# Kernel optimization log

Hardware: AMD Instinct MI355X
Metric: run time of the kernel (lower is better)

Reference implementation:

```python
import jax, jax.numpy as jnp
import numpy as np

EMBED_DIM = 1024
NUM_HEADS = 16
D_K = EMBED_DIM // NUM_HEADS
GAMMA = 1.0


def setup_inputs() -> dict:
    key = jax.random.key(0)
    ks = jax.random.split(key, 5)
    B, N, E = 2, 2048, EMBED_DIM
    scale = 1.0 / np.sqrt(E)
    x = jax.random.normal(ks[0], (B, N, E), dtype=jnp.float32)
    Wq = jax.random.normal(ks[1], (E, E), dtype=jnp.float32) * scale
    Wk = jax.random.normal(ks[2], (E, E), dtype=jnp.float32) * scale
    Wv = jax.random.normal(ks[3], (E, E), dtype=jnp.float32) * scale
    Wo = jax.random.normal(ks[4], (E, E), dtype=jnp.float32) * scale
    mask = jnp.ones((B, N), dtype=jnp.int32)
    return {"x": x, "Wq": Wq, "Wk": Wk, "Wv": Wv, "Wo": Wo, "mask": mask}


def _split_heads(t):
    B, N, E = t.shape
    return t.reshape(B, N, NUM_HEADS, D_K).transpose(0, 2, 1, 3)  # [B,H,N,dk]


def reference(x, Wq, Wk, Wv, Wo, mask):
    B, N, E = x.shape
    # Linear layers (bias=False): y = x @ W.T
    q = _split_heads(x @ Wq.T)
    k = _split_heads(x @ Wk.T)
    v = _split_heads(x @ Wv.T)
    # Squared L2 distance via ||q||^2 + ||k||^2 - 2 q.k (same math as (q-k)^2.sum,
    # without materializing the [B,H,N,N,dk] diff tensor).
    q_sq = jnp.sum(q * q, axis=-1)  # [B,H,N]
    k_sq = jnp.sum(k * k, axis=-1)  # [B,H,N]
    qk = jnp.einsum('bhqd,bhkd->bhqk', q, k)
    sq_dist = jnp.maximum(q_sq[..., :, None] + k_sq[..., None, :] - 2.0 * qk, 0.0)
    similarity = jnp.exp(-GAMMA * sq_dist)  # [B,H,N,N]
    # mask.unsqueeze(1).unsqueeze(2): broadcast over heads and query dim
    mask_exp = mask[:, None, None, :]  # [B,1,1,N]
    similarity = jnp.where(mask_exp == 0, jnp.float32(-1e9), similarity)
    attn = jax.nn.softmax(similarity, axis=-1)
    # dropout p=0.0 (eval) -> identity
    out = jnp.einsum('bhqk,bhkd->bhqd', attn, v)
    out = out.transpose(0, 2, 1, 3).reshape(B, N, E)
    return out @ Wo.T
```

## Files before the change

kernel.cpp:

```cpp
#include <hip/hip_runtime.h>
#include <hip/hip_bf16.h>


using bf16x8 = __attribute__((ext_vector_type(8))) __bf16;
using f32x4  = __attribute__((ext_vector_type(4))) float;
using f32x16 = __attribute__((ext_vector_type(16))) float;

typedef const __attribute__((address_space(1))) void* gas_t;
typedef __attribute__((address_space(3))) void* las_t;

#define C_LOG2E 1.4426950408889634f
#define TWO_C   2.8853900817779268f
#define NEG_INV_4C (-0.17328679513998632f)

#if __has_builtin(__builtin_amdgcn_exp2f)
#define EXP2(x) __builtin_amdgcn_exp2f(x)
#else
#define EXP2(x) __expf((x) * 0.6931471805599453f)
#endif

static __device__ __forceinline__ unsigned short f2bf(float x) {
  union { float f; unsigned u; } c; c.f = x;
  unsigned u = c.u;
  u += 0x7fffu + ((u >> 16) & 1u);
  return (unsigned short)(u >> 16);
}
static __device__ __forceinline__ float bf2f(unsigned short b) {
  union { unsigned u; float f; } c; c.u = ((unsigned)b) << 16;
  return c.f;
}
static __device__ __forceinline__ unsigned cvt_pk_bf16(float lo, float hi) {
  unsigned r;
  asm("v_cvt_pk_bf16_f32 %0, %1, %2" : "=v"(r) : "v"(lo), "v"(hi));
  return r;
}
static __device__ __forceinline__ void permlane32_swap(unsigned &a, unsigned &b) {
#if __has_builtin(__builtin_amdgcn_permlane32_swap)
  auto r = __builtin_amdgcn_permlane32_swap(a, b, false, false);
  a = r[0]; b = r[1];
#else
  asm("v_permlane32_swap_b32 %0, %1" : "+v"(a), "+v"(b));
#endif
}

__global__ __launch_bounds__(256)
void cvt_all(const float* __restrict__ x,  const float* __restrict__ wq,
             const float* __restrict__ wk, const float* __restrict__ wv,
             const float* __restrict__ wo,
             unsigned short* __restrict__ xbf, unsigned short* __restrict__ Wbf) {
  const int idx = blockIdx.x * 256 + threadIdx.x;
  const float* src; unsigned short* dst; int off;
  if (idx < 1048576) { src = x; dst = xbf; off = idx; }
  else {
    const int r = idx - 1048576;
    const int w = r >> 18;
    off = r & 262143;
    src = (w == 0) ? wq : (w == 1) ? wk : (w == 2) ? wv : wo;
    dst = Wbf + (size_t)w * 1048576u;
  }
  const float4 v = ((const float4*)src)[off];
  ushort4 o;
  o.x = f2bf(v.x); o.y = f2bf(v.y); o.z = f2bf(v.z); o.w = f2bf(v.w);
  ((ushort4*)dst)[off] = o;
}

__global__ __launch_bounds__(256)
void gemm_bt(const unsigned short* __restrict__ A,
             const unsigned short* __restrict__ Bt,
             void* __restrict__ out0, int Kdim, int mode) {
  __shared__ unsigned short As[2][4096];
  __shared__ unsigned short Bs[2][4096];
  const int t  = threadIdx.x;
  const int m0 = blockIdx.x * 128;
  const int n0 = blockIdx.y * 128;
  const int srow = t >> 2;
  const int scol = (t & 3) * 8;
  const unsigned short* pA = A  + (size_t)(m0 + srow) * Kdim + scol;
  const unsigned short* pB = Bt + (size_t)(n0 + srow) * Kdim + scol;
  const size_t rowskip = (size_t)64 * Kdim;

  const int wave = t >> 6, lane = t & 63;
  const int wm = (wave >> 1) * 64, wn = (wave & 1) * 64;
  const int fr = lane & 15, fg = lane >> 4;
  const int aoff = (wm + fr) * 32 + fg * 8;
  const int boff = (wn + fr) * 32 + fg * 8;

  f32x4 acc[4][4];
#pragma unroll
  for (int mi = 0; mi < 4; ++mi)
#pragma unroll
    for (int ni = 0; ni < 4; ++ni)
      acc[mi][ni] = (f32x4){0.f, 0.f, 0.f, 0.f};

#define GSTAGE(bi, kk)                                                                                  \
  do {                                                                                                  \
    const int kc = (kk) * 32;                                                                           \
    __builtin_amdgcn_global_load_lds((gas_t)(const void*)(pA + kc),           (las_t)(void*)(As[bi] + t * 8),        16, 0, 0); \
    __builtin_amdgcn_global_load_lds((gas_t)(const void*)(pA + kc + rowskip), (las_t)(void*)(As[bi] + 2048 + t * 8), 16, 0, 0); \
    __builtin_amdgcn_global_load_lds((gas_t)(const void*)(pB + kc),           (las_t)(void*)(Bs[bi] + t * 8),        16, 0, 0); \
    __builtin_amdgcn_global_load_lds((gas_t)(const void*)(pB + kc + rowskip), (las_t)(void*)(Bs[bi] + 2048 + t * 8), 16, 0, 0); \
  } while (0)

  const int NK = Kdim >> 5;
  GSTAGE(0, 0);
  __syncthreads();

  for (int ks = 0; ks < NK; ++ks) {
    const int cur = ks & 1;
    if (ks + 1 < NK) GSTAGE(cur ^ 1, ks + 1);

    bf16x8 af[4], bfr[4];
#pragma unroll
    for (int mi = 0; mi < 4; ++mi) af[mi]  = *(const bf16x8*)(As[cur] + aoff + mi * 512);
#pragma unroll
    for (int ni = 0; ni < 4; ++ni) bfr[ni] = *(const bf16x8*)(Bs[cur] + boff + ni * 512);
#pragma unroll
    for (int mi = 0; mi < 4; ++mi)
#pragma unroll
      for (int ni = 0; ni < 4; ++ni)
        acc[mi][ni] = __builtin_amdgcn_mfma_f32_16x16x32_bf16(af[mi], bfr[ni], acc[mi][ni], 0, 0, 0);
    __syncthreads();
  }
#undef GSTAGE

#pragma unroll
  for (int mi = 0; mi < 4; ++mi) {
    const int gm = m0 + wm + mi * 16 + fg * 4;
#pragma unroll
    for (int ni = 0; ni < 4; ++ni) {
      const int gn = n0 + wn + ni * 16 + fr;
      if (mode == 0) {
        unsigned short* outw = (unsigned short*)out0;
        const int z = gn >> 10, col = gn & 1023;
        if (z < 2) {
          const float sc = (z == 0) ? TWO_C : 1.0f;
          unsigned short* dst = outw + (size_t)z * 4194304u;
#pragma unroll
          for (int r = 0; r < 4; ++r)
            dst[(size_t)(gm + r) * 1024 + col] = f2bf(acc[mi][ni][r] * sc);
        } else {
          ushort4 o4;
          o4.x = f2bf(acc[mi][ni][0]); o4.y = f2bf(acc[mi][ni][1]);
          o4.z = f2bf(acc[mi][ni][2]); o4.w = f2bf(acc[mi][ni][3]);
          const int bb = gm >> 11, nn = gm & 2047;
          const int hh = col >> 6, dd = col & 63;
          unsigned short* vt = outw + (size_t)2 * 4194304u;
          *(ushort4*)(vt + ((size_t)((bb * 16 + hh) * 64 + dd)) * 2048 + nn) = o4;
        }
      } else {
        float* dst = (float*)out0;
#pragma unroll
        for (int r = 0; r < 4; ++r)
          dst[(size_t)(gm + r) * 1024 + gn] = acc[mi][ni][r];
      }
    }
  }
}

__global__ __launch_bounds__(256)
void rowsq_kernel(const unsigned short* __restrict__ Qbf,
                  const unsigned short* __restrict__ Kbf,
                  const int* __restrict__ mask,
                  float* __restrict__ qsqp, float* __restrict__ ksqp,
                  float* __restrict__ maskf) {
  const int tid = blockIdx.x * 256 + threadIdx.x;
  const int kpath = blockIdx.y;
  const unsigned short* src = (kpath == 0) ? Qbf : Kbf;
  const int bh = tid >> 11, n = tid & 2047;
  const int b = bh >> 4, h = bh & 15;
  const unsigned short* row = src + (size_t)(b * 2048 + n) * 1024 + h * 64;
  float s = 0.f;
#pragma unroll
  for (int c = 0; c < 64; c += 4) {
    ushort4 v = *(const ushort4*)(row + c);
    float f0 = bf2f(v.x), f1 = bf2f(v.y), f2 = bf2f(v.z), f3 = bf2f(v.w);
    s += f0 * f0 + f1 * f1 + f2 * f2 + f3 * f3;
  }
  if (kpath == 0) {
    qsqp[tid] = s * NEG_INV_4C;
  } else {
    ksqp[tid] = s * (-C_LOG2E);
    if (tid < 4096) maskf[tid] = (mask[tid] == 0) ? 0.f : 1.f;
  }
}

__global__ __launch_bounds__(256)
void prep_kernel(const unsigned short* __restrict__ Vt,
                 const float* __restrict__ maskf,
                 const float* __restrict__ ksqp,
                 float* __restrict__ FullVm,
                 float* __restrict__ den_base,
                 float* __restrict__ kmaxb) {
  const int bh = blockIdx.x;
  const int b = bh >> 4;
  const int wave = threadIdx.x >> 6, lane = threadIdx.x & 63;
  for (int dr = wave * 16; dr < wave * 16 + 16; ++dr) {
    const unsigned short* row = Vt + ((size_t)bh * 64 + dr) * 2048 + lane * 32;
    const float* mrow = maskf + b * 2048 + lane * 32;
    float s = 0.f;
#pragma unroll
    for (int c = 0; c < 32; c += 4) {
      ushort4 v = *(const ushort4*)(row + c);
      float4 m = *(const float4*)(mrow + c);
      s += bf2f(v.x) * m.x + bf2f(v.y) * m.y + bf2f(v.z) * m.z + bf2f(v.w) * m.w;
    }
#pragma unroll
    for (int off = 32; off >= 1; off >>= 1) s += __shfl_xor(s, off);
    if (lane == 0) FullVm[bh * 64 + dr] = s;
  }
  if (wave == 0) {
    const float* kp = ksqp + bh * 2048 + lane;
    float mx = -3.0e38f;
    for (int c = 0; c < 2048; c += 64) mx = fmaxf(mx, kp[c]);
#pragma unroll
    for (int off = 32; off >= 1; off >>= 1) mx = fmaxf(mx, __shfl_xor(mx, off));
    if (lane == 0) kmaxb[bh] = mx;
  }
  if (wave == 1 && (bh == 0 || bh == 16)) {
    const float* mrow = maskf + b * 2048 + lane;
    float s = 0.f;
    for (int c = 0; c < 2048; c += 64) s += mrow[c];
#pragma unroll
    for (int off = 32; off >= 1; off >>= 1) s += __shfl_xor(s, off);
    if (lane == 0) den_base[b] = s;
  }
}

__global__ __launch_bounds__(256)
void attn_kernel(const unsigned short* __restrict__ Qbf,
                 const unsigned short* __restrict__ Kbf,
                 const unsigned short* __restrict__ Vt,
                 const float* __restrict__ qsqp,
                 const float* __restrict__ ksqp,
                 const float* __restrict__ maskf,
                 const float* __restrict__ FullVm,
                 const float* __restrict__ den_base,
                 const float* __restrict__ kmaxb,
                 unsigned short* __restrict__ Obf) {
  __shared__ unsigned short Ks[2][4096];
  __shared__ float Obuf[2][32][64];
  __shared__ float Dbuf[2][64];

  const int bh = blockIdx.x;
  const int b = bh >> 4, h = bh & 15;
  const int t = threadIdx.x;
  const int wave = t >> 6, lane = t & 63;
  const int qg = wave >> 1, hf = wave & 1;
  const int li = lane & 31, hi = lane >> 5;
  const int q0 = blockIdx.y * 64 + qg * 32;
  const int qrow = q0 + li;

  const unsigned short* Qr = Qbf + (size_t)(b * 2048 + qrow) * 1024 + h * 64 + hi * 8;
  bf16x8 qf[4];
#pragma unroll
  for (int dblk = 0; dblk < 4; ++dblk) qf[dblk] = *(const bf16x8*)(Qr + dblk * 16);

  const float qsl = qsqp[bh * 2048 + qrow];
  const float thr = -14.0f - qsl - kmaxb[bh];

  const unsigned short* Kbase = Kbf + (size_t)b * 2048 * 1024 + h * 64;
  const unsigned short* VtB = Vt + (size_t)bh * 64 * 2048;

  const int p0 = t,        r0 = p0 >> 3, c0 = (p0 & 7) ^ (r0 & 7);
  const int p1 = 256 + t,  r1 = p1 >> 3, c1 = (p1 & 7) ^ (r1 & 7);

  f32x16 oa0, oa1;
#pragma unroll
  for (int r = 0; r < 16; ++r) { oa0[r] = 0.f; oa1[r] = 0.f; }
  float den = 0.f;

#define STAGE(bi, tj)                                                                               \
  do {                                                                                              \
    const int j0s = (tj) * 64;                                                                      \
    __builtin_amdgcn_global_load_lds((gas_t)(const void*)(Kbase + (size_t)(j0s + r0) * 1024 + c0 * 8), \
                                     (las_t)(void*)(Ks[bi] + p0 * 8), 16, 0, 0);                    \
    __builtin_amdgcn_global_load_lds((gas_t)(const void*)(Kbase + (size_t)(j0s + r1) * 1024 + c1 * 8), \
                                     (las_t)(void*)(Ks[bi] + p1 * 8), 16, 0, 0);                    \
  } while (0)

  STAGE(0, 0);
  __syncthreads();

  const int jw = hf * 32;
  const int krow = jw + li;
  const int ksw = krow & 7;

  for (int tj = 0; tj < 32; ++tj) {
    const int cur = tj & 1;
    if (tj + 1 < 32) STAGE(cur ^ 1, tj + 1);

    const unsigned short* Krow = Ks[cur] + krow * 64;
    f32x16 st;
#pragma unroll
    for (int r = 0; r < 16; ++r) st[r] = 0.f;
#pragma unroll
    for (int dblk = 0; dblk < 4; ++dblk) {
      const bf16x8 kf = *(const bf16x8*)(Krow + ((dblk * 2 + hi) ^ ksw) * 8);
      st = __builtin_amdgcn_mfma_f32_32x32x16_bf16(kf, qf[dblk], st, 0, 0, 0);
    }

    const float a0 = fmaxf(fmaxf(st[0], st[1]), st[2]);
    const float a1 = fmaxf(fmaxf(st[3], st[4]), st[5]);
    const float a2 = fmaxf(fmaxf(st[6], st[7]), st[8]);
    const float a3 = fmaxf(fmaxf(st[9], st[10]), st[11]);
    const float a4 = fmaxf(fmaxf(st[12], st[13]), st[14]);
    const float a5 = fmaxf(fmaxf(a0, a1), st[15]);
    const float a6 = fmaxf(fmaxf(a2, a3), a4);
    const float lmax = fmaxf(a5, a6);

    if (__any(lmax > thr)) {
      const int j0 = tj * 64 + jw;
      const float* ksb2 = ksqp + bh * 2048 + j0 + 4 * hi;
      const float* mfb2 = maskf + b * 2048 + j0 + 4 * hi;
      const float4 kq0 = *(const float4*)(ksb2);
      const float4 kq1 = *(const float4*)(ksb2 + 8);
      const float4 kq2 = *(const float4*)(ksb2 + 16);
      const float4 kq3 = *(const float4*)(ksb2 + 24);
      const float4 mf0 = *(const float4*)(mfb2);
      const float4 mf1 = *(const float4*)(mfb2 + 8);
      const float4 mf2 = *(const float4*)(mfb2 + 16);
      const float4 mf3 = *(const float4*)(mfb2 + 24);
      const float kqa[16] = {kq0.x, kq0.y, kq0.z, kq0.w, kq1.x, kq1.y, kq1.z, kq1.w,
                             kq2.x, kq2.y, kq2.z, kq2.w, kq3.x, kq3.y, kq3.z, kq3.w};
      const float mfa[16] = {mf0.x, mf0.y, mf0.z, mf0.w, mf1.x, mf1.y, mf1.z, mf1.w,
                             mf2.x, mf2.y, mf2.z, mf2.w, mf3.x, mf3.y, mf3.z, mf3.w};
      float dsv[16];
#pragma unroll
      for (int r = 0; r < 16; ++r) {
        const float z = __builtin_fminf(st[r] + qsl + kqa[r], 0.f);
        const float s = EXP2(z);
        float pl = __builtin_fmaf(s, 1.f / 120.f, 1.f / 24.f);
        pl = __builtin_fmaf(s, pl, 1.f / 6.f);
        pl = __builtin_fmaf(s, pl, 0.5f);
        pl = __builtin_fmaf(s, pl, 1.f);
        const float d_ = s * pl * mfa[r];
        dsv[r] = d_;
        den += d_;
      }

      unsigned u00 = cvt_pk_bf16(dsv[0],  dsv[1]);
      unsigned u01 = cvt_pk_bf16(dsv[2],  dsv[3]);
      unsigned u10 = cvt_pk_bf16(dsv[4],  dsv[5]);
      unsigned u11 = cvt_pk_bf16(dsv[6],  dsv[7]);
      unsigned u20 = cvt_pk_bf16(dsv[8],  dsv[9]);
      unsigned u21 = cvt_pk_bf16(dsv[10], dsv[11]);
      unsigned u30 = cvt_pk_bf16(dsv[12], dsv[13]);
      unsigned u31 = cvt_pk_bf16(dsv[14], dsv[15]);
      permlane32_swap(u00, u10);
      permlane32_swap(u01, u11);
      permlane32_swap(u20, u30);
      permlane32_swap(u21, u31);
      union { unsigned u[4]; bf16x8 v; } pf0, pf1;
      pf0.u[0] = u00; pf0.u[1] = u01; pf0.u[2] = u10; pf0.u[3] = u11;
      pf1.u[0] = u20; pf1.u[1] = u21; pf1.u[2] = u30; pf1.u[3] = u31;

#pragma unroll
      for (int dh = 0; dh < 2; ++dh) {
        const unsigned short* Vrow = VtB + (size_t)(dh * 32 + li) * 2048 + tj * 64;
        const bf16x8 vf0 = *(const bf16x8*)(Vrow + (hf * 4 + 0 + hi) * 8);
        const bf16x8 vf1 = *(const bf16x8*)(Vrow + (hf * 4 + 2 + hi) * 8);
        if (dh == 0) {
          oa0 = __builtin_amdgcn_mfma_f32_32x32x16_bf16(vf0, pf0.v, oa0, 0, 0, 0);
          oa0 = __builtin_amdgcn_mfma_f32_32x32x16_bf16(vf1, pf1.v, oa0, 0, 0, 0);
        } else {
          oa1 = __builtin_amdgcn_mfma_f32_32x32x16_bf16(vf0, pf0.v, oa1, 0, 0, 0);
          oa1 = __builtin_amdgcn_mfma_f32_32x32x16_bf16(vf1, pf1.v, oa1, 0, 0, 0);
        }
      }
    }

    __syncthreads();
  }
#undef STAGE

  den += __shfl_xor(den, 32);

  if (hf == 1) {
#pragma unroll
    for (int r = 0; r < 16; ++r) {
      Obuf[qg][r][lane]      = oa0[r];
      Obuf[qg][16 + r][lane] = oa1[r];
    }
    Dbuf[qg][lane] = den;
  }
  __syncthreads();
  if (hf == 0) {
    const float inv = 1.f / (den_base[b] + den + Dbuf[qg][lane]);
    const float* fvm = FullVm + bh * 64;
    unsigned short* orow = Obf + (size_t)(b * 2048 + qrow) * 1024 + h * 64;
#pragma unroll
    for (int dh = 0; dh < 2; ++dh)
#pragma unroll
      for (int w = 0; w < 4; ++w) {
        float v0, v1, v2, v3;
        if (dh == 0) {
          v0 = oa0[4 * w];     v1 = oa0[4 * w + 1];
          v2 = oa0[4 * w + 2]; v3 = oa0[4 * w + 3];
        } else {
          v0 = oa1[4 * w];     v1 = oa1[4 * w + 1];
          v2 = oa1[4 * w + 2]; v3 = oa1[4 * w + 3];
        }
        v0 += Obuf[qg][dh * 16 + 4 * w + 0][lane];
        v1 += Obuf[qg][dh * 16 + 4 * w + 1][lane];
        v2 += Obuf[qg][dh * 16 + 4 * w + 2][lane];
        v3 += Obuf[qg][dh * 16 + 4 * w + 3][lane];
        const float4 fv = *(const float4*)(fvm + dh * 32 + w * 8 + hi * 4);
        ushort4 o4;
        o4.x = f2bf((v0 + fv.x) * inv);
        o4.y = f2bf((v1 + fv.y) * inv);
        o4.z = f2bf((v2 + fv.z) * inv);
        o4.w = f2bf((v3 + fv.w) * inv);
        *(ushort4*)(orow + dh * 32 + w * 8 + hi * 4) = o4;
      }
  }
}

extern "C" void kernel_launch(void* const* d_in, const int* in_sizes, int n_in,
                              void* d_out, int out_size, void* d_ws, size_t ws_size,
                              hipStream_t stream) {
  const float* x  = (const float*)d_in[0];
  const float* Wq = (const float*)d_in[1];
  const float* Wk = (const float*)d_in[2];
  const float* Wv = (const float*)d_in[3];
  const float* Wo = (const float*)d_in[4];
  const int* mask = (const int*)d_in[5];

  unsigned short* ws = (unsigned short*)d_ws;
  const size_t SZ = 4194304;
  unsigned short* xbf = ws;
  unsigned short* Wbf = ws + SZ;
  unsigned short* Qbf = ws + 2 * SZ;
  unsigned short* Kbf = ws + 3 * SZ;
  unsigned short* Vt  = ws + 4 * SZ;
  unsigned short* Obf = ws + 5 * SZ;
  float* qsqp = (float*)(ws + 6 * SZ);
  float* ksqp = qsqp + 65536;
  float* maskf = ksqp + 65536;
  float* FullVm = maskf + 4096;
  float* den_base = FullVm + 2048;
  float* kmaxb = den_base + 2;

  cvt_all<<<8192, 256, 0, stream>>>(x, Wq, Wk, Wv, Wo, xbf, Wbf);

  gemm_bt<<<dim3(32, 24), 256, 0, stream>>>(xbf, Wbf, Qbf, 1024, 0);

  rowsq_kernel<<<dim3(256, 2), 256, 0, stream>>>(Qbf, Kbf, mask, qsqp, ksqp, maskf);

  prep_kernel<<<32, 256, 0, stream>>>(Vt, maskf, ksqp, FullVm, den_base, kmaxb);

  attn_kernel<<<dim3(32, 32), 256, 0, stream>>>(Qbf, Kbf, Vt, qsqp, ksqp, maskf,
                                                FullVm, den_base, kmaxb, Obf);

  gemm_bt<<<dim3(32, 8), 256, 0, stream>>>(Obf, Wbf + 3145728, d_out, 1024, 1);
}
```

Baseline: 123.7 us.

## Triple-buffer GEMM and attention K loads; split prep kernel across key chunks

The GEMM and attention loops move from double to triple-buffered LDS staging. Each iteration now has a single vmcnt-limited wait plus barrier, so two tiles stay in flight and the trailing __syncthreads per iteration is gone. The prep kernel is split into 8 key chunks per head (256 blocks instead of 32). Its partial sums and max are combined with atomics into buffers that rowsq_kernel now zero-initialises, and the max uses atomicMin on float bits, which relies on the values being non-positive. Attention's output-reduction scratch now aliases the K buffers so the extra stage does not add LDS, at the cost of an extra barrier before reuse.

Result: faster. 116.6 us (-5.7%).

```diff
diff --git a/kernel.cpp b/kernel.cpp
--- a/kernel.cpp
+++ b/kernel.cpp
@@ -42,6 +42,12 @@
   asm("v_permlane32_swap_b32 %0, %1" : "+v"(a), "+v"(b));
 #endif
 }
+
+#define SYNC_VM(N)                                                           \
+  do {                                                                       \
+    asm volatile("s_waitcnt vmcnt(" #N ") lgkmcnt(0)\n\ts_barrier" ::: "memory"); \
+    __builtin_amdgcn_sched_barrier(0);                                       \
+  } while (0)
 
 __global__ __launch_bounds__(256)
 void cvt_all(const float* __restrict__ x,  const float* __restrict__ wq,
@@ -68,8 +74,8 @@
 void gemm_bt(const unsigned short* __restrict__ A,
              const unsigned short* __restrict__ Bt,
              void* __restrict__ out0, int Kdim, int mode) {
-  __shared__ unsigned short As[2][4096];
-  __shared__ unsigned short Bs[2][4096];
+  __shared__ unsigned short As[3][4096];
+  __shared__ unsigned short Bs[3][4096];
   const int t  = threadIdx.x;
   const int m0 = blockIdx.x * 128;
   const int n0 = blockIdx.y * 128;
@@ -103,11 +109,12 @@
 
   const int NK = Kdim >> 5;
   GSTAGE(0, 0);
-  __syncthreads();
+  GSTAGE(1, 1);
 
   for (int ks = 0; ks < NK; ++ks) {
-    const int cur = ks & 1;
-    if (ks + 1 < NK) GSTAGE(cur ^ 1, ks + 1);
+    const int cur = ks % 3;
+    if (ks + 1 < NK) SYNC_VM(4); else SYNC_VM(0);
+    if (ks + 2 < NK) GSTAGE((ks + 2) % 3, ks + 2);
 
     bf16x8 af[4], bfr[4];
 #pragma unroll
@@ -119,7 +126,6 @@
 #pragma unroll
       for (int ni = 0; ni < 4; ++ni)
         acc[mi][ni] = __builtin_amdgcn_mfma_f32_16x16x32_bf16(af[mi], bfr[ni], acc[mi][ni], 0, 0, 0);
-    __syncthreads();
   }
 #undef GSTAGE
 
@@ -162,7 +168,10 @@
                   const unsigned short* __restrict__ Kbf,
                   const int* __restrict__ mask,
                   float* __restrict__ qsqp, float* __restrict__ ksqp,
-                  float* __restrict__ maskf) {
+                  float* __restrict__ maskf,
+                  float* __restrict__ FullVm,
+                  float* __restrict__ den_base,
+                  unsigned* __restrict__ kmax_bits) {
   const int tid = blockIdx.x * 256 + threadIdx.x;
   const int kpath = blockIdx.y;
   const unsigned short* src = (kpath == 0) ? Qbf : Kbf;
@@ -178,6 +187,9 @@
   }
   if (kpath == 0) {
     qsqp[tid] = s * NEG_INV_4C;
+    if (tid < 2048) FullVm[tid] = 0.f;
+    if (tid < 32) kmax_bits[tid] = 0xFF800000u;
+    if (tid < 2) den_base[tid] = 0.f;
   } else {
     ksqp[tid] = s * (-C_LOG2E);
     if (tid < 4096) maskf[tid] = (mask[tid] == 0) ? 0.f : 1.f;
@@ -185,44 +197,37 @@
 }
 
 __global__ __launch_bounds__(256)
-void prep_kernel(const unsigned short* __restrict__ Vt,
-                 const float* __restrict__ maskf,
-                 const float* __restrict__ ksqp,
-                 float* __restrict__ FullVm,
-                 float* __restrict__ den_base,
-                 float* __restrict__ kmaxb) {
-  const int bh = blockIdx.x;
+void prep2_kernel(const unsigned short* __restrict__ Vt,
+                  const float* __restrict__ maskf,
+                  const float* __restrict__ ksqp,
+                  float* __restrict__ FullVm,
+                  float* __restrict__ den_base,
+                  unsigned* __restrict__ kmax_bits) {
+  const int bh = blockIdx.x, c = blockIdx.y;
   const int b = bh >> 4;
   const int wave = threadIdx.x >> 6, lane = threadIdx.x & 63;
+  const int k0 = c * 256;
+  const float4 mv = *(const float4*)(maskf + b * 2048 + k0 + lane * 4);
+#pragma unroll 4
   for (int dr = wave * 16; dr < wave * 16 + 16; ++dr) {
-    const unsigned short* row = Vt + ((size_t)bh * 64 + dr) * 2048 + lane * 32;
-    const float* mrow = maskf + b * 2048 + lane * 32;
-    float s = 0.f;
-#pragma unroll
-    for (int c = 0; c < 32; c += 4) {
-      ushort4 v = *(const ushort4*)(row + c);
-      float4 m = *(const float4*)(mrow + c);
-      s += bf2f(v.x) * m.x + bf2f(v.y) * m.y + bf2f(v.z) * m.z + bf2f(v.w) * m.w;
-    }
+    const ushort4 v = *(const ushort4*)(Vt + ((size_t)bh * 64 + dr) * 2048 + k0 + lane * 4);
+    float s = bf2f(v.x) * mv.x + bf2f(v.y) * mv.y + bf2f(v.z) * mv.z + bf2f(v.w) * mv.w;
 #pragma unroll
     for (int off = 32; off >= 1; off >>= 1) s += __shfl_xor(s, off);
-    if (lane == 0) FullVm[bh * 64 + dr] = s;
+    if (lane == 0) atomicAdd(&FullVm[bh * 64 + dr], s);
   }
   if (wave == 0) {
-    const float* kp = ksqp + bh * 2048 + lane;
-    float mx = -3.0e38f;
-    for (int c = 0; c < 2048; c += 64) mx = fmaxf(mx, kp[c]);
+    const float4 kq = *(const float4*)(ksqp + bh * 2048 + k0 + lane * 4);
+    float mx = fmaxf(fmaxf(kq.x, kq.y), fmaxf(kq.z, kq.w));
 #pragma unroll
     for (int off = 32; off >= 1; off >>= 1) mx = fmaxf(mx, __shfl_xor(mx, off));
-    if (lane == 0) kmaxb[bh] = mx;
-  }
-  if (wave == 1 && (bh == 0 || bh == 16)) {
-    const float* mrow = maskf + b * 2048 + lane;
-    float s = 0.f;
-    for (int c = 0; c < 2048; c += 64) s += mrow[c];
+    if (lane == 0) atomicMin(&kmax_bits[bh], __float_as_uint(mx));
+  }
+  if (wave == 1 && (bh & 15) == 0) {
+    float s = mv.x + mv.y + mv.z + mv.w;
 #pragma unroll
     for (int off = 32; off >= 1; off >>= 1) s += __shfl_xor(s, off);
-    if (lane == 0) den_base[b] = s;
+    if (lane == 0) atomicAdd(&den_base[b], s);
   }
 }
 
@@ -237,9 +242,7 @@
                  const float* __restrict__ den_base,
                  const float* __restrict__ kmaxb,
                  unsigned short* __restrict__ Obf) {
-  __shared__ unsigned short Ks[2][4096];
-  __shared__ float Obuf[2][32][64];
-  __shared__ float Dbuf[2][64];
+  __shared__ unsigned short Ks[3][4096];
 
   const int bh = blockIdx.x;
   const int b = bh >> 4, h = bh & 15;
@@ -279,15 +282,16 @@
   } while (0)
 
   STAGE(0, 0);
-  __syncthreads();
+  STAGE(1, 1);
 
   const int jw = hf * 32;
   const int krow = jw + li;
   const int ksw = krow & 7;
 
   for (int tj = 0; tj < 32; ++tj) {
-    const int cur = tj & 1;
-    if (tj + 1 < 32) STAGE(cur ^ 1, tj + 1);
+    const int cur = tj % 3;
+    if (tj + 1 < 32) SYNC_VM(2); else SYNC_VM(0);
+    if (tj + 2 < 32) STAGE((tj + 2) % 3, tj + 2);
 
     const unsigned short* Krow = Ks[cur] + krow * 64;
     f32x16 st;
@@ -368,24 +372,25 @@
         }
       }
     }
-
-    __syncthreads();
   }
 #undef STAGE
 
   den += __shfl_xor(den, 32);
 
+  __syncthreads();
+  float* Obuf = (float*)&Ks[0][0];
+  float* Dbuf = (float*)&Ks[0][0] + 4096;
   if (hf == 1) {
 #pragma unroll
     for (int r = 0; r < 16; ++r) {
-      Obuf[qg][r][lane]      = oa0[r];
-      Obuf[qg][16 + r][lane] = oa1[r];
+      Obuf[(qg * 32 + r) * 64 + lane]      = oa0[r];
+      Obuf[(qg * 32 + 16 + r) * 64 + lane] = oa1[r];
     }
-    Dbuf[qg][lane] = den;
+    Dbuf[qg * 64 + lane] = den;
   }
   __syncthreads();
   if (hf == 0) {
-    const float inv = 1.f / (den_base[b] + den + Dbuf[qg][lane]);
+    const float inv = 1.f / (den_base[b] + den + Dbuf[qg * 64 + lane]);
     const float* fvm = FullVm + bh * 64;
     unsigned short* orow = Obf + (size_t)(b * 2048 + qrow) * 1024 + h * 64;
 #pragma unroll
@@ -400,10 +405,9 @@
           v0 = oa1[4 * w];     v1 = oa1[4 * w + 1];
           v2 = oa1[4 * w + 2]; v3 = oa1[4 * w + 3];
         }
-        v0 += Obuf[qg][dh * 16 + 4 * w + 0][lane];
-        v1 += Obuf[qg][dh * 16 + 4 * w + 1][lane];
-        v2 += Obuf[qg][dh * 16 + 4 * w + 2][lane];
-        v3 += Obuf[qg][dh * 16 + 4 * w + 3][lane];
+        const int sbase = (qg * 32 + dh * 16 + 4 * w) * 64 + lane;
+        v0 += Obuf[sbase];       v1 += Obuf[sbase + 64];
+        v2 += Obuf[sbase + 128]; v3 += Obuf[sbase + 192];
         const float4 fv = *(const float4*)(fvm + dh * 32 + w * 8 + hi * 4);
         ushort4 o4;
         o4.x = f2bf((v0 + fv.x) * inv);
@@ -444,9 +448,11 @@
 
   gemm_bt<<<dim3(32, 24), 256, 0, stream>>>(xbf, Wbf, Qbf, 1024, 0);
 
-  rowsq_kernel<<<dim3(256, 2), 256, 0, stream>>>(Qbf, Kbf, mask, qsqp, ksqp, maskf);
-
-  prep_kernel<<<32, 256, 0, stream>>>(Vt, maskf, ksqp, FullVm, den_base, kmaxb);
+  rowsq_kernel<<<dim3(256, 2), 256, 0, stream>>>(Qbf, Kbf, mask, qsqp, ksqp, maskf,
+                                                 FullVm, den_base, (unsigned*)kmaxb);
+
+  prep2_kernel<<<dim3(32, 8), 256, 0, stream>>>(Vt, maskf, ksqp, FullVm, den_base,
+                                                (unsigned*)kmaxb);
 
   attn_kernel<<<dim3(32, 32), 256, 0, stream>>>(Qbf, Kbf, Vt, qsqp, ksqp, maskf,
                                                 FullVm, den_base, kmaxb, Obf);
```
